# Kernel tuning notes

Hardware: AMD Instinct MI355X
Metric: run time of the kernel (lower is better)

Reference implementation:

```python
import jax, jax.numpy as jnp
import numpy as np

N, F_IN, F_OUT, K = 4096, 32, 32, 2
NEG_SLOPE = 0.2
MASK_VAL = -9e15


def _sparse_mat(kv, km, density=0.01):
    vals = jax.random.normal(kv, (N, N), dtype=jnp.float32)
    mask = jax.random.uniform(km, (N, N)) < density
    return vals * mask


def setup_inputs() -> dict:
    key = jax.random.key(0)
    ks = jax.random.split(key, 12)
    x = jax.random.normal(ks[0], (N, F_IN), dtype=jnp.float32)
    Ld = _sparse_mat(ks[1], ks[2])
    Lu = _sparse_mat(ks[3], ks[4])
    P = jax.random.normal(ks[5], (N, N), dtype=jnp.float32) / np.sqrt(N)
    W1 = jax.random.normal(ks[6], (K, F_IN, F_OUT), dtype=jnp.float32) * 0.1
    W2 = jax.random.normal(ks[7], (K, F_IN, F_OUT), dtype=jnp.float32) * 0.1
    W0 = jax.random.normal(ks[8], (F_IN, F_OUT), dtype=jnp.float32) * 0.1
    att1 = jax.random.normal(ks[9], (2 * F_OUT * K, 1), dtype=jnp.float32) * 0.1
    att2 = jax.random.normal(ks[10], (2 * F_OUT * K, 1), dtype=jnp.float32) * 0.1
    return {"x": x, "Ld": Ld, "Lu": Lu, "P": P, "W1": W1, "W2": W2,
            "W0": W0, "att1": att1, "att2": att2}


def _branch(x, L, W, att):
    # W: [K, F_in, F_out]; precompute x @ W[k] for all k -> [K, N, F_out]
    Kk, _, Fo = W.shape
    xw = jnp.einsum('nf,kfo->kno', x, W)
    # torch.cat([x@W[k]], dim=1) == transpose+reshape of xw
    xcat = jnp.transpose(xw, (1, 0, 2)).reshape(x.shape[0], Kk * Fo)
    d = Fo * Kk
    e = xcat @ att[:d] + (xcat @ att[d:]).T            # [N, N]
    e = jax.nn.leaky_relu(e, negative_slope=NEG_SLOPE)
    e = jnp.where(L != 0, e, MASK_VAL)
    alpha = jax.nn.softmax(e, axis=1)                   # row softmax, no dropout (eval)
    z = alpha @ xw[0]
    a = alpha
    for k in range(1, Kk):
        a = a @ L
        z = z + a @ xw[k]
    return z


def reference(x, Ld, Lu, P, W1, W2, W0, att1, att2):
    z1 = _branch(x, Ld, W1, att1)
    z2 = _branch(x, Lu, W2, att2)
    x0 = P @ (x @ W0)
    return z1 + z2 + x0
```

## Files before the change

kernel.cpp:

```cpp
#include <hip/hip_runtime.h>
#include <hip/hip_bf16.h>

#define NN 4096
#define CAP 128
#define KS 8

typedef __attribute__((ext_vector_type(8))) short bf16x8;
typedef __attribute__((ext_vector_type(4))) float f32x4;

__device__ __forceinline__ float lrelu(float v) { return v >= 0.f ? v : 0.2f * v; }

__device__ __forceinline__ ushort f2bu(float f) {
    unsigned u = __float_as_uint(f);
    return (ushort)((u + 0x7FFFu + ((u >> 16) & 1u)) >> 16);
}

__global__ __launch_bounds__(256) void k_prep(
    const float* __restrict__ x,
    const float* __restrict__ W1, const float* __restrict__ W2,
    const float* __restrict__ W0,
    const float* __restrict__ att1, const float* __restrict__ att2,
    float* __restrict__ xwA1, float* __restrict__ xwB1,
    float* __restrict__ xwA2, float* __restrict__ xwB2,
    float* __restrict__ a1, float* __restrict__ b1,
    float* __restrict__ a2, float* __restrict__ b2,
    __hip_bfloat16* __restrict__ Bt)
{
    __shared__ float wl[5120];
    __shared__ float xs[256];
    const int t = threadIdx.x;
    for (int i = t; i < 2048; i += 256) { wl[i] = W1[i]; wl[2048 + i] = W2[i]; }
    for (int i = t; i < 1024; i += 256) wl[4096 + i] = W0[i];
    const int rowBase = blockIdx.x * 8;
    xs[t] = x[rowBase * 32 + t];
    __syncthreads();

    const int o = t & 31, r = t >> 5;
    const int row = rowBase + r;
    const float* xr = &xs[r * 32];
    float vA1 = 0.f, vB1 = 0.f, vA2 = 0.f, vB2 = 0.f, v0 = 0.f;
#pragma unroll
    for (int f = 0; f < 32; ++f) {
        const float xv = xr[f];
        vA1 += xv * wl[f * 32 + o];
        vB1 += xv * wl[1024 + f * 32 + o];
        vA2 += xv * wl[2048 + f * 32 + o];
        vB2 += xv * wl[3072 + f * 32 + o];
        v0  += xv * wl[4096 + f * 32 + o];
    }
    xwA1[row * 32 + o] = vA1;
    xwB1[row * 32 + o] = vB1;
    xwA2[row * 32 + o] = vA2;
    xwB2[row * 32 + o] = vB2;
    ((ushort*)Bt)[(size_t)o * NN + row] = f2bu(v0);

    float pa1 = vA1 * att1[o]      + vB1 * att1[32 + o];
    float pb1 = vA1 * att1[64 + o] + vB1 * att1[96 + o];
    float pa2 = vA2 * att2[o]      + vB2 * att2[32 + o];
    float pb2 = vA2 * att2[64 + o] + vB2 * att2[96 + o];
#pragma unroll
    for (int m = 1; m <= 16; m <<= 1) {
        pa1 += __shfl_xor(pa1, m); pb1 += __shfl_xor(pb1, m);
        pa2 += __shfl_xor(pa2, m); pb2 += __shfl_xor(pb2, m);
    }
    if (o == 0) { a1[row] = pa1; b1[row] = pb1; a2[row] = pa2; b2[row] = pb2; }
}

__global__ __launch_bounds__(256) void k_scan6(
    const float* __restrict__ L,
    const float* __restrict__ xwB, const float* __restrict__ xwA,
    const float* __restrict__ aA, const float* __restrict__ bA,
    int2* __restrict__ csrv, int* __restrict__ cntArr,
    float* __restrict__ u)
{
    const int row = blockIdx.x;
    int2* csrB = csrv + (size_t)row * CAP;

    __shared__ int   sidx[CAP];
    __shared__ float sval[CAP];
    __shared__ int   wcnt[16];
    __shared__ float red[256];
    __shared__ float rpart[8];
    const int t = threadIdx.x;
    const int lane = t & 63, w = t >> 6;

    const float4* L4 = (const float4*)(L + (size_t)row * NN);
    float4 v[4];
#pragma unroll
    for (int it = 0; it < 4; ++it) v[it] = L4[it * 256 + t];

    const unsigned long long lt = (1ull << lane) - 1ull;

    unsigned long long M0[4], M1[4], M2[4], M3[4];
    int tots[4];
#pragma unroll
    for (int it = 0; it < 4; ++it) {
        M0[it] = __ballot(v[it].x != 0.f);
        M1[it] = __ballot(v[it].y != 0.f);
        M2[it] = __ballot(v[it].z != 0.f);
        M3[it] = __ballot(v[it].w != 0.f);
        tots[it] = __popcll(M0[it]) + __popcll(M1[it]) + __popcll(M2[it]) + __popcll(M3[it]);
    }
    if (lane == 0) {
        int4 tv; tv.x = tots[0]; tv.y = tots[1]; tv.z = tots[2]; tv.w = tots[3];
        *(int4*)&wcnt[w * 4] = tv;
    }
    __syncthreads();

    const int4 ca = *(const int4*)&wcnt[0];
    const int4 cb = *(const int4*)&wcnt[4];
    const int4 cc = *(const int4*)&wcnt[8];
    const int4 cd = *(const int4*)&wcnt[12];
    const int cs[16] = {ca.x, ca.y, ca.z, ca.w, cb.x, cb.y, cb.z, cb.w,
                        cc.x, cc.y, cc.z, cc.w, cd.x, cd.y, cd.z, cd.w};
    int total = 0;
#pragma unroll
    for (int k2 = 0; k2 < 16; ++k2) total += cs[k2];
    int base = 0;
#pragma unroll
    for (int k2 = 0; k2 < 16; ++k2) base += (k2 < (w << 2)) ? cs[k2] : 0;

    const int cnt  = min(total, CAP);
    const int cp16 = min((cnt + 15) & ~15, CAP);

#pragma unroll
    for (int it = 0; it < 4; ++it) {
        const float vx = v[it].x, vy = v[it].y, vz = v[it].z, vw = v[it].w;
        const int p0 = __popcll(M0[it]), p1 = __popcll(M1[it]), p2 = __popcll(M2[it]);
        const int c0 = (it * 256 + t) * 4;
        int s;
        s = base + __popcll(M0[it] & lt);
        if (vx != 0.f && s < CAP) { sidx[s] = c0;     sval[s] = vx; }
        s = base + p0 + __popcll(M1[it] & lt);
        if (vy != 0.f && s < CAP) { sidx[s] = c0 + 1; sval[s] = vy; }
        s = base + p0 + p1 + __popcll(M2[it] & lt);
        if (vz != 0.f && s < CAP) { sidx[s] = c0 + 2; sval[s] = vz; }
        s = base + p0 + p1 + p2 + __popcll(M3[it] & lt);
        if (vw != 0.f && s < CAP) { sidx[s] = c0 + 3; sval[s] = vw; }
        base += p0 + p1 + p2 + __popcll(M3[it]);
    }
    if (t >= cnt && t < cp16) { sidx[t] = 0; sval[t] = 0.f; }
    __syncthreads();

    const float ai = aA[row];
    const int myidx = (t < cp16) ? sidx[t] : 0;
    const float e = (t < cnt) ? lrelu(ai + bA[myidx]) : -1e30f;
    float m = e;
#pragma unroll
    for (int mm = 1; mm <= 32; mm <<= 1) m = fmaxf(m, __shfl_xor(m, mm));
    if (lane == 0) rpart[w] = m;
    __syncthreads();
    m = fmaxf(fmaxf(rpart[0], rpart[1]), fmaxf(rpart[2], rpart[3]));
    const float wgt = (t < cnt) ? __expf(e - m) : 0.f;
    float ss = wgt;
#pragma unroll
    for (int mm = 1; mm <= 32; mm <<= 1) ss += __shfl_xor(ss, mm);
    if (lane == 0) rpart[4 + w] = ss;
    __syncthreads();
    const float ssum = rpart[4] + rpart[5] + rpart[6] + rpart[7];
    const float inv = (cnt > 0) ? 1.f / ssum : 0.f;
    if (t < cp16) { int2 eo; eo.x = myidx; eo.y = __float_as_int(wgt * inv); csrB[t] = eo; }
    if (t == 0) cntArr[row] = cnt;

    const int o = t & 31, g = t >> 5;
    float acc = 0.f;
    const int nPair = cp16 >> 4;
    if (nPair > 0) {
        float vA0 = sval[g],      vA1 = sval[g + 8];
        float xA0 = xwB[(size_t)sidx[g] * 32 + o];
        float xA1 = xwB[(size_t)sidx[g + 8] * 32 + o];
        for (int j = 1; j < nPair; ++j) {
            const int sB = g + 16 * j;
            const float vB0 = sval[sB],  vB1 = sval[sB + 8];
            const float xB0 = xwB[(size_t)sidx[sB] * 32 + o];
            const float xB1 = xwB[(size_t)sidx[sB + 8] * 32 + o];
            acc += vA0 * xA0 + vA1 * xA1;
            vA0 = vB0; xA0 = xB0; vA1 = vB1; xA1 = xB1;
        }
        acc += vA0 * xA0 + vA1 * xA1;
    }
    red[t] = acc;
    __syncthreads();
    if (t < 32) {
        float tot2 = 0.f;
#pragma unroll
        for (int g2 = 0; g2 < 8; ++g2) tot2 += red[g2 * 32 + t];
        u[(size_t)row * 32 + t] = tot2 + xwA[(size_t)row * 32 + t];
    }
}

__global__ __launch_bounds__(256) void k_accum(
    const int2* __restrict__ csrv, const int* __restrict__ cntArr,
    const float* __restrict__ u1, const float* __restrict__ u2,
    const float* __restrict__ partial, float* __restrict__ outp)
{
    __shared__ int2 sle[4][2 * CAP];
    const int w = threadIdx.x >> 6, lane = threadIdx.x & 63;
    const int row = blockIdx.x * 4 + w;
    const int o = lane & 31, g = lane >> 5;
    int2* se = sle[w];
    float total = 0.f;

    int cp[2];
#pragma unroll
    for (int br = 0; br < 2; ++br) {
        const int cnt = cntArr[br * NN + row];
        cp[br] = min((cnt + 15) & ~15, CAP);
        const int2* ci = csrv + ((size_t)br * NN + row) * CAP;
        if (lane < cp[br])      se[br * CAP + lane]      = ci[lane];
        if (lane + 64 < cp[br]) se[br * CAP + lane + 64] = ci[lane + 64];
    }

#pragma unroll
    for (int br = 0; br < 2; ++br) {
        const float* U = br ? u2 : u1;
        float acc = 0.f;
        const int nb = cp[br] >> 3;
        for (int j = 0; j < nb; ++j) {
            float wv[4], uv[4];
#pragma unroll
            for (int q = 0; q < 4; ++q) {
                const int2 e = se[br * CAP + 8 * j + 2 * q + g];
                wv[q] = __int_as_float(e.y);
                uv[q] = U[(size_t)e.x * 32 + o];
            }
#pragma unroll
            for (int q = 0; q < 4; ++q) acc += wv[q] * uv[q];
        }
        acc += __shfl_xor(acc, 32);
        total += acc;
    }

    if (lane < 32) {
#pragma unroll
        for (int p = 0; p < KS; ++p)
            total += partial[(size_t)p * NN * 32 + (size_t)row * 32 + o];
        outp[(size_t)row * 32 + o] = total;
    }
}

__global__ __launch_bounds__(256) void k_pgemm2(
    const float* __restrict__ P, const ushort* __restrict__ Bt,
    float* __restrict__ partial)
{
    const int t = threadIdx.x;
    const int lane = t & 63, w = t >> 6;
    const int gw = blockIdx.x * 4 + w;
    const int mt = gw & 255;
    const int ks = gw >> 8;
    const int m0 = mt * 16;
    const int r  = lane & 15;
    const int kq = lane >> 4;

    const float*  pa  = P  + (size_t)(m0 + r) * NN + ks * 512 + kq * 8;
    const ushort* pb0 = Bt + (size_t)r        * NN + ks * 512 + kq * 8;
    const ushort* pb1 = Bt + (size_t)(16 + r) * NN + ks * 512 + kq * 8;

    f32x4 acc0 = {0.f, 0.f, 0.f, 0.f};
    f32x4 acc1 = {0.f, 0.f, 0.f, 0.f};

#pragma unroll 4
    for (int kk = 0; kk < 16; ++kk) {
        const float4 a0 = *(const float4*)(pa + kk * 32);
        const float4 a1 = *(const float4*)(pa + kk * 32 + 4);
        const bf16x8 b0 = *(const bf16x8*)(pb0 + kk * 32);
        const bf16x8 b1 = *(const bf16x8*)(pb1 + kk * 32);
        bf16x8 a;
        a[0] = (short)f2bu(a0.x); a[1] = (short)f2bu(a0.y);
        a[2] = (short)f2bu(a0.z); a[3] = (short)f2bu(a0.w);
        a[4] = (short)f2bu(a1.x); a[5] = (short)f2bu(a1.y);
        a[6] = (short)f2bu(a1.z); a[7] = (short)f2bu(a1.w);
        acc0 = __builtin_amdgcn_mfma_f32_16x16x32_bf16(a, b0, acc0, 0, 0, 0);
        acc1 = __builtin_amdgcn_mfma_f32_16x16x32_bf16(a, b1, acc1, 0, 0, 0);
    }

    float* out = partial + ((size_t)ks * NN + m0 + kq * 4) * 32;
#pragma unroll
    for (int rr = 0; rr < 4; ++rr) {
        out[rr * 32 + r]      = acc0[rr];
        out[rr * 32 + 16 + r] = acc1[rr];
    }
}

extern "C" void kernel_launch(void* const* d_in, const int* in_sizes, int n_in,
                              void* d_out, int out_size, void* d_ws, size_t ws_size,
                              hipStream_t stream) {
    (void)in_sizes; (void)n_in; (void)out_size; (void)ws_size;
    const float* x    = (const float*)d_in[0];
    const float* Ld   = (const float*)d_in[1];
    const float* Lu   = (const float*)d_in[2];
    const float* P    = (const float*)d_in[3];
    const float* W1   = (const float*)d_in[4];
    const float* W2   = (const float*)d_in[5];
    const float* W0   = (const float*)d_in[6];
    const float* att1 = (const float*)d_in[7];
    const float* att2 = (const float*)d_in[8];

    float* ws = (float*)d_ws;
    float* xwA1 = ws;
    float* xwB1 = ws + 131072;
    float* xwA2 = ws + 262144;
    float* xwB2 = ws + 393216;
    float* u1   = ws + 524288;
    float* u2   = ws + 655360;
    float* a1   = ws + 786432;
    float* b1   = ws + 790528;
    float* a2   = ws + 794624;
    float* b2   = ws + 798720;
    float* partial = ws + 802816;
    __hip_bfloat16* Bt = (__hip_bfloat16*)(ws + 1851392);
    int2* csrv = (int2*)(ws + 1916928);
    int*  cnt  = (int*)(ws + 4014080);

    k_prep<<<512, 256, 0, stream>>>(x, W1, W2, W0, att1, att2,
                                    xwA1, xwB1, xwA2, xwB2, a1, b1, a2, b2, Bt);
    k_scan6<<<NN, 256, 0, stream>>>(Ld, xwB1, xwA1, a1, b1,
                                    csrv, cnt, u1);
    k_scan6<<<NN, 256, 0, stream>>>(Lu, xwB2, xwA2, a2, b2,
                                    csrv + (size_t)NN * CAP, cnt + NN, u2);
    k_pgemm2<<<512, 256, 0, stream>>>(P, (const ushort*)Bt, partial);
    k_accum<<<NN / 4, 256, 0, stream>>>(csrv, cnt, u1, u2, partial,
                                        (float*)d_out);
}
```

Measured before the change: 231.1 us.

## Merge both scan launches and P-GEMM into one heterogeneous-block kernel

Combines the two per-branch scan kernels and the bf16 MFMA P-GEMM into a single launch. Block IDs below 512 do the GEMM tile work, and the rest handle scan rows for either Ld or Lu, selected by block index. This removes two kernel launches and the tail bubbles between them, and lets the compute-bound GEMM blocks overlap with the memory-bound scan blocks. In exchange, every block carries the union of register and shared-memory usage, which may reduce occupancy for the GEMM path.

After: 224.2 us. 1.03x faster.

```diff
diff --git a/kernel.cpp b/kernel.cpp
--- a/kernel.cpp
+++ b/kernel.cpp
@@ -4,6 +4,7 @@
 #define NN 4096
 #define CAP 128
 #define KS 8
+#define PGB 512
 
 typedef __attribute__((ext_vector_type(8))) short bf16x8;
 typedef __attribute__((ext_vector_type(4))) float f32x4;
@@ -66,23 +67,76 @@
     if (o == 0) { a1[row] = pa1; b1[row] = pb1; a2[row] = pa2; b2[row] = pb2; }
 }
 
-__global__ __launch_bounds__(256) void k_scan6(
-    const float* __restrict__ L,
-    const float* __restrict__ xwB, const float* __restrict__ xwA,
-    const float* __restrict__ aA, const float* __restrict__ bA,
+__global__ __launch_bounds__(256) void k_fused(
+    const float* __restrict__ Ld, const float* __restrict__ Lu,
+    const float* __restrict__ xwB1, const float* __restrict__ xwB2,
+    const float* __restrict__ xwA1, const float* __restrict__ xwA2,
+    const float* __restrict__ a1, const float* __restrict__ b1,
+    const float* __restrict__ a2, const float* __restrict__ b2,
     int2* __restrict__ csrv, int* __restrict__ cntArr,
-    float* __restrict__ u)
+    float* __restrict__ u1, float* __restrict__ u2,
+    const float* __restrict__ P, const ushort* __restrict__ Bt,
+    float* __restrict__ partial)
 {
-    const int row = blockIdx.x;
-    int2* csrB = csrv + (size_t)row * CAP;
-
     __shared__ int   sidx[CAP];
     __shared__ float sval[CAP];
     __shared__ int   wcnt[16];
     __shared__ float red[256];
     __shared__ float rpart[8];
+
+    const int bid = blockIdx.x;
     const int t = threadIdx.x;
     const int lane = t & 63, w = t >> 6;
+
+    if (bid < PGB) {
+        const int gw = bid * 4 + w;
+        const int mt = gw & 255;
+        const int ks = gw >> 8;
+        const int m0 = mt * 16;
+        const int r  = lane & 15;
+        const int kq = lane >> 4;
+
+        const float*  pa  = P  + (size_t)(m0 + r) * NN + ks * 512 + kq * 8;
+        const ushort* pb0 = Bt + (size_t)r        * NN + ks * 512 + kq * 8;
+        const ushort* pb1 = Bt + (size_t)(16 + r) * NN + ks * 512 + kq * 8;
+
+        f32x4 acc0 = {0.f, 0.f, 0.f, 0.f};
+        f32x4 acc1 = {0.f, 0.f, 0.f, 0.f};
+
+#pragma unroll 4
+        for (int kk = 0; kk < 16; ++kk) {
+            const float4 a0 = *(const float4*)(pa + kk * 32);
+            const float4 a1v = *(const float4*)(pa + kk * 32 + 4);
+            const bf16x8 b0 = *(const bf16x8*)(pb0 + kk * 32);
+            const bf16x8 b1v = *(const bf16x8*)(pb1 + kk * 32);
+            bf16x8 a;
+            a[0] = (short)f2bu(a0.x); a[1] = (short)f2bu(a0.y);
+            a[2] = (short)f2bu(a0.z); a[3] = (short)f2bu(a0.w);
+            a[4] = (short)f2bu(a1v.x); a[5] = (short)f2bu(a1v.y);
+            a[6] = (short)f2bu(a1v.z); a[7] = (short)f2bu(a1v.w);
+            acc0 = __builtin_amdgcn_mfma_f32_16x16x32_bf16(a, b0, acc0, 0, 0, 0);
+            acc1 = __builtin_amdgcn_mfma_f32_16x16x32_bf16(a, b1v, acc1, 0, 0, 0);
+        }
+
+        float* out = partial + ((size_t)ks * NN + m0 + kq * 4) * 32;
+#pragma unroll
+        for (int rr = 0; rr < 4; ++rr) {
+            out[rr * 32 + r]      = acc0[rr];
+            out[rr * 32 + 16 + r] = acc1[rr];
+        }
+        return;
+    }
+
+    const int sb  = bid - PGB;
+    const int br  = sb >> 12;
+    const int row = sb & (NN - 1);
+    const float* L   = br ? Lu : Ld;
+    const float* xwB = br ? xwB2 : xwB1;
+    const float* xwA = br ? xwA2 : xwA1;
+    const float* aA  = br ? a2 : a1;
+    const float* bA  = br ? b2 : b1;
+    int2* csrB = csrv + ((size_t)br * NN + row) * CAP;
+    float* u   = br ? u2 : u1;
 
     const float4* L4 = (const float4*)(L + (size_t)row * NN);
     float4 v[4];
@@ -160,7 +214,7 @@
     const float ssum = rpart[4] + rpart[5] + rpart[6] + rpart[7];
     const float inv = (cnt > 0) ? 1.f / ssum : 0.f;
     if (t < cp16) { int2 eo; eo.x = myidx; eo.y = __float_as_int(wgt * inv); csrB[t] = eo; }
-    if (t == 0) cntArr[row] = cnt;
+    if (t == 0) cntArr[br * NN + row] = cnt;
 
     const int o = t & 31, g = t >> 5;
     float acc = 0.f;
@@ -239,49 +293,6 @@
     }
 }
 
-__global__ __launch_bounds__(256) void k_pgemm2(
-    const float* __restrict__ P, const ushort* __restrict__ Bt,
-    float* __restrict__ partial)
-{
-    const int t = threadIdx.x;
-    const int lane = t & 63, w = t >> 6;
-    const int gw = blockIdx.x * 4 + w;
-    const int mt = gw & 255;
-    const int ks = gw >> 8;
-    const int m0 = mt * 16;
-    const int r  = lane & 15;
-    const int kq = lane >> 4;
-
-    const float*  pa  = P  + (size_t)(m0 + r) * NN + ks * 512 + kq * 8;
-    const ushort* pb0 = Bt + (size_t)r        * NN + ks * 512 + kq * 8;
-    const ushort* pb1 = Bt + (size_t)(16 + r) * NN + ks * 512 + kq * 8;
-
-    f32x4 acc0 = {0.f, 0.f, 0.f, 0.f};
-    f32x4 acc1 = {0.f, 0.f, 0.f, 0.f};
-
-#pragma unroll 4
-    for (int kk = 0; kk < 16; ++kk) {
-        const float4 a0 = *(const float4*)(pa + kk * 32);
-        const float4 a1 = *(const float4*)(pa + kk * 32 + 4);
-        const bf16x8 b0 = *(const bf16x8*)(pb0 + kk * 32);
-        const bf16x8 b1 = *(const bf16x8*)(pb1 + kk * 32);
-        bf16x8 a;
-        a[0] = (short)f2bu(a0.x); a[1] = (short)f2bu(a0.y);
-        a[2] = (short)f2bu(a0.z); a[3] = (short)f2bu(a0.w);
-        a[4] = (short)f2bu(a1.x); a[5] = (short)f2bu(a1.y);
-        a[6] = (short)f2bu(a1.z); a[7] = (short)f2bu(a1.w);
-        acc0 = __builtin_amdgcn_mfma_f32_16x16x32_bf16(a, b0, acc0, 0, 0, 0);
-        acc1 = __builtin_amdgcn_mfma_f32_16x16x32_bf16(a, b1, acc1, 0, 0, 0);
-    }
-
-    float* out = partial + ((size_t)ks * NN + m0 + kq * 4) * 32;
-#pragma unroll
-    for (int rr = 0; rr < 4; ++rr) {
-        out[rr * 32 + r]      = acc0[rr];
-        out[rr * 32 + 16 + r] = acc1[rr];
-    }
-}
-
 extern "C" void kernel_launch(void* const* d_in, const int* in_sizes, int n_in,
                               void* d_out, int out_size, void* d_ws, size_t ws_size,
                               hipStream_t stream) {
@@ -314,11 +325,9 @@
 
     k_prep<<<512, 256, 0, stream>>>(x, W1, W2, W0, att1, att2,
                                     xwA1, xwB1, xwA2, xwB2, a1, b1, a2, b2, Bt);
-    k_scan6<<<NN, 256, 0, stream>>>(Ld, xwB1, xwA1, a1, b1,
-                                    csrv, cnt, u1);
-    k_scan6<<<NN, 256, 0, stream>>>(Lu, xwB2, xwA2, a2, b2,
-                                    csrv + (size_t)NN * CAP, cnt + NN, u2);
-    k_pgemm2<<<512, 256, 0, stream>>>(P, (const ushort*)Bt, partial);
+    k_fused<<<PGB + 2 * NN, 256, 0, stream>>>(Ld, Lu, xwB1, xwB2, xwA1, xwA2,
+                                              a1, b1, a2, b2, csrv, cnt, u1, u2,
+                                              P, (const ushort*)Bt, partial);
     k_accum<<<NN / 4, 256, 0, stream>>>(csrv, cnt, u1, u2, partial,
                                         (float*)d_out);
 }
```
